# Kernel tuning notes

Hardware: AMD Instinct MI355X
Metric: run time of the kernel (lower is better)

The kernel has to match this reference:

```python
import jax, jax.numpy as jnp
import numpy as np

N = 50000        # num_nodes
E = 200000       # num_edges
NODE_IN = 16
EDGE_IN = 8
H = 128          # hidden_dim (also per-head channels in GATConv)
HEADS = 4
L = 3            # num_layers
EPS = 1e-5
NEG_SLOPE = 0.2  # PyG GATConv default


def layer_norm(x, g, b):
    mu = jnp.mean(x, axis=-1, keepdims=True)
    v = jnp.var(x, axis=-1, keepdims=True)
    return (x - mu) * jax.lax.rsqrt(v + EPS) * g + b


def batch_norm_eval(x, g, b, rm, rv):
    return (x - rm) * jax.lax.rsqrt(rv + EPS) * g + b


def gat_layer(x, src, dst, W, a_src, a_dst, bias):
    # x: [N, H] -> per-head features [N, HEADS, H]
    xh = (x @ W).reshape(N, HEADS, H)
    al_src = jnp.sum(xh * a_src, axis=-1)  # [N, HEADS]
    al_dst = jnp.sum(xh * a_dst, axis=-1)  # [N, HEADS]
    alpha = jax.nn.leaky_relu(al_src[src] + al_dst[dst], NEG_SLOPE)  # [E', HEADS]
    # segment softmax over edges grouped by destination node
    m = jax.ops.segment_max(alpha, dst, num_segments=N)
    e = jnp.exp(alpha - m[dst])
    s = jax.ops.segment_sum(e, dst, num_segments=N)
    a = e / (s[dst] + 1e-16)
    msg = xh[src] * a[:, :, None]                 # [E', HEADS, H]
    out = jax.ops.segment_sum(msg, dst, num_segments=N)  # [N, HEADS, H]
    return jnp.mean(out, axis=1) + bias           # concat=False -> head mean


def setup_inputs() -> dict:
    key = jax.random.key(0)
    ks = jax.random.split(key, 24)
    s = 0.1
    inp = {
        "x": jax.random.normal(ks[0], (N, NODE_IN), jnp.float32),
        "edge_index": jax.random.randint(ks[1], (2, E), 0, N, jnp.int32),
        "edge_attr": jax.random.normal(ks[2], (E, EDGE_IN), jnp.float32),
        "shock_mask_nodes": jax.random.randint(ks[3], (N,), 0, 2, jnp.int32),
        # node encoder
        "enc_w": jax.random.normal(ks[4], (NODE_IN + 2, H), jnp.float32) * s,
        "enc_b": jnp.zeros((H,), jnp.float32),
        "enc_ln_g": jnp.ones((H,), jnp.float32),
        "enc_ln_b": jnp.zeros((H,), jnp.float32),
        # GAT layers (stacked over L)
        "gat_w": jax.random.normal(ks[5], (L, H, HEADS * H), jnp.float32) * s,
        "gat_att_src": jax.random.normal(ks[6], (L, HEADS, H), jnp.float32) * s,
        "gat_att_dst": jax.random.normal(ks[7], (L, HEADS, H), jnp.float32) * s,
        "gat_bias": jnp.zeros((L, H), jnp.float32),
        # BatchNorm (eval mode: running stats)
        "bn_g": jnp.ones((L, H), jnp.float32),
        "bn_b": jnp.zeros((L, H), jnp.float32),
        "bn_mean": jax.random.normal(ks[8], (L, H), jnp.float32) * 0.01,
        "bn_var": jnp.ones((L, H), jnp.float32),
        # edge MLP: (2H + EDGE_IN) -> H -> H//2 -> 1
        "em1_w": jax.random.normal(ks[9], (2 * H + EDGE_IN, H), jnp.float32) * s,
        "em1_b": jnp.zeros((H,), jnp.float32),
        "em_ln_g": jnp.ones((H,), jnp.float32),
        "em_ln_b": jnp.zeros((H,), jnp.float32),
        "em2_w": jax.random.normal(ks[10], (H, H // 2), jnp.float32) * s,
        "em2_b": jnp.zeros((H // 2,), jnp.float32),
        "em3_w": jax.random.normal(ks[11], (H // 2, 1), jnp.float32) * s,
        "em3_b": jnp.zeros((1,), jnp.float32),
    }
    return inp


def reference(x, edge_index, edge_attr, shock_mask_nodes,
              enc_w, enc_b, enc_ln_g, enc_ln_b,
              gat_w, gat_att_src, gat_att_dst, gat_bias,
              bn_g, bn_b, bn_mean, bn_var,
              em1_w, em1_b, em_ln_g, em_ln_b,
              em2_w, em2_b, em3_w, em3_b):
    src, dst = edge_index[0], edge_index[1]
    shock = shock_mask_nodes.astype(jnp.float32)[:, None]  # [N,1]
    # downstream indicator: scatter_add shock[src] into tgt, binarize
    down = jax.ops.segment_sum(shock[src, 0], dst, num_segments=N)
    down = (down > 0).astype(jnp.float32)[:, None]
    xa = jnp.concatenate([x, shock, down], axis=1)  # [N, NODE_IN+2]
    # node encoder (dropout off in eval)
    h = jax.nn.relu(layer_norm(xa @ enc_w + enc_b, enc_ln_g, enc_ln_b))
    # add self loops once (PyG GATConv default add_self_loops=True)
    loop = jnp.arange(N, dtype=src.dtype)
    src_sl = jnp.concatenate([src, loop])
    dst_sl = jnp.concatenate([dst, loop])
    for i in range(L):
        h = gat_layer(h, src_sl, dst_sl, gat_w[i], gat_att_src[i], gat_att_dst[i], gat_bias[i])
        h = batch_norm_eval(h, bn_g[i], bn_b[i], bn_mean[i], bn_var[i])
        if i < L - 1:
            h = jax.nn.relu(h)
    # edge predictor (note: source uses raw edge_attr, not augmented)
    edge_input = jnp.concatenate([h[src], h[dst], edge_attr], axis=1)  # [E, 2H+EDGE_IN]
    z = jax.nn.relu(layer_norm(edge_input @ em1_w + em1_b, em_ln_g, em_ln_b))
    z = jax.nn.relu(z @ em2_w + em2_b)
    delta = (z @ em3_w + em3_b)[:, 0]  # [E]
    return delta
```

## Files before the change

kernel.cpp:

```cpp
#include <hip/hip_runtime.h>
#include <hip/hip_bf16.h>


#define N_NODES 50000
#define N_EDGES 200000
#define ETOT    (N_EDGES + N_NODES)
#define HID     128
#define LN_EPS  1e-5f
#define NEG     0.2f

typedef __hip_bfloat16 bf16;
typedef __attribute__((ext_vector_type(8))) short v8s;
typedef __attribute__((ext_vector_type(4))) float v4f;
#define MFMA(a, b, c) __builtin_amdgcn_mfma_f32_16x16x32_bf16(a, b, c, 0, 0, 0)

__device__ __forceinline__ float b2f(unsigned short s) {
    return __uint_as_float(((unsigned int)s) << 16);
}
__device__ __forceinline__ unsigned short f2b(float f) {
    __hip_bfloat16 h = __float2bfloat16(f);
    return *reinterpret_cast<unsigned short*>(&h);
}
__device__ __forceinline__ unsigned int pack2(float a, float b) {
    return (unsigned int)f2b(a) | ((unsigned int)f2b(b) << 16);
}
__device__ __forceinline__ float pread(const void* p, size_t i, int isbf) {
    if (isbf) return b2f(((const unsigned short*)p)[i]);
    return ((const float*)p)[i];
}

__global__ void k_fill(float* out, int n, float v) {
    int i = blockIdx.x * blockDim.x + threadIdx.x;
    if (i < n) out[i] = v;
}

__global__ void k_detect(const unsigned short* __restrict__ xbuf,
                         int* __restrict__ flag) {
    int sane = 0;
    for (int j = threadIdx.x; j < 4096; j += 64) {
        unsigned short v = xbuf[2 * j];
        int e = (v >> 7) & 0xFF;
        if (v == 0 || (e > 96 && e < 160)) sane++;
    }
    for (int off = 32; off > 0; off >>= 1) sane += __shfl_down(sane, off);
    if (threadIdx.x == 0) flag[0] = (sane * 10 >= 4096 * 9) ? 1 : 0;
}

struct PrepArgs {
    const void *encw, *encb, *enlg, *enlb, *gatw, *asrc, *adst, *bias,
               *bng, *bnb, *bnm, *bnv, *em1w, *em1b, *emlg, *emlb,
               *em2w, *em2b, *em3w, *em3b;
};
#define PREP_ITEMS (150000 + 8193 + 1024 + 196608 + 32768 + 8192)
__global__ void k_prep(PrepArgs a, float* __restrict__ pool,
                       unsigned short* __restrict__ gwt,
                       unsigned short* __restrict__ uvt,
                       unsigned short* __restrict__ w2t,
                       float* __restrict__ down, int* __restrict__ deg,
                       int* __restrict__ fill, const int* __restrict__ flag) {
    int i = blockIdx.x * 256 + threadIdx.x;
    int bf = flag[0];
    if (i < 150000) {
        int which = i / 50000, idx = i - which * 50000;
        if (which == 0) down[idx] = 0.f;
        else if (which == 1) deg[idx] = 0;
        else fill[idx] = 0;
        return;
    }
    i -= 150000;
    if (i < 8193) {
        const void* s; int off;
        if      (i < 2304) { s = a.encw; off = 0;    }
        else if (i < 2432) { s = a.encb; off = 2304; }
        else if (i < 2560) { s = a.enlg; off = 2432; }
        else if (i < 2688) { s = a.enlb; off = 2560; }
        else if (i < 4224) { s = a.asrc; off = 2688; }
        else if (i < 5760) { s = a.adst; off = 4224; }
        else if (i < 6144) { s = a.bias; off = 5760; }
        else if (i < 6528) { s = a.bng;  off = 6144; }
        else if (i < 6912) { s = a.bnb;  off = 6528; }
        else if (i < 7296) { s = a.bnm;  off = 6912; }
        else if (i < 7680) { s = a.bnv;  off = 7296; }
        else if (i < 7808) { s = a.em1b; off = 7680; }
        else if (i < 7936) { s = a.emlg; off = 7808; }
        else if (i < 8064) { s = a.emlb; off = 7936; }
        else if (i < 8128) { s = a.em2b; off = 8064; }
        else if (i < 8192) { s = a.em3w; off = 8128; }
        else               { s = a.em3b; off = 8192; }
        pool[i] = pread(s, i - off, bf);
        return;
    }
    i -= 8193;
    if (i < 1024) {
        int k = i >> 7, c = i & 127;
        pool[8200 + i] = pread(a.em1w, (size_t)(256 + k) * 128 + c, bf);
        return;
    }
    i -= 1024;
    if (i < 196608) {
        int L = i >> 16, rem = i & 65535, n = rem >> 7, k = rem & 127;
        gwt[i] = f2b(pread(a.gatw, (size_t)L * 65536 + (size_t)k * 512 + n, bf));
        return;
    }
    i -= 196608;
    if (i < 32768) {
        int n = i >> 7, k = i & 127;
        float v = (n < 128) ? pread(a.em1w, (size_t)k * 128 + n, bf)
                            : pread(a.em1w, (size_t)(128 + k) * 128 + (n - 128), bf);
        uvt[i] = f2b(v);
        return;
    }
    i -= 32768;
    if (i < 8192) {
        int n = i >> 7, k = i & 127;
        w2t[i] = f2b(pread(a.em2w, (size_t)k * 64 + n, bf));
    }
}

__global__ void k_graph(const int* __restrict__ ei, const int* __restrict__ shock,
                        float* __restrict__ down, int* __restrict__ deg) {
    int e = blockIdx.x * blockDim.x + threadIdx.x;
    if (e < ETOT) {
        int d = (e < N_EDGES) ? ei[N_EDGES + e] : (e - N_EDGES);
        atomicAdd(&deg[d], 1);
        if (e < N_EDGES && shock[ei[e]] != 0) down[d] = 1.f;
    }
}

__global__ __launch_bounds__(1024) void k_scan(
        const int* __restrict__ deg, int* __restrict__ row_start) {
    __shared__ int wsum[16];
    __shared__ int wexcl[16];
    const int PER = 49;
    int t = threadIdx.x, lane = t & 63, wid = t >> 6;
    int base = t * PER;
    int tot = 0;
    for (int i = 0; i < PER; i++) {
        int idx = base + i;
        if (idx < N_NODES) tot += deg[idx];
    }
    int inc = tot;
#pragma unroll
    for (int off = 1; off < 64; off <<= 1) {
        int v = __shfl_up(inc, off);
        if (lane >= off) inc += v;
    }
    if (lane == 63) wsum[wid] = inc;
    __syncthreads();
    if (wid == 0) {
        int wv = (lane < 16) ? wsum[lane] : 0;
        int winc = wv;
#pragma unroll
        for (int off = 1; off < 16; off <<= 1) {
            int v = __shfl_up(winc, off);
            if (lane >= off) winc += v;
        }
        if (lane < 16) wexcl[lane] = winc - wv;
    }
    __syncthreads();
    int run = wexcl[wid] + (inc - tot);
    for (int i = 0; i < PER; i++) {
        int idx = base + i;
        if (idx < N_NODES) {
            row_start[idx] = run;
            run += deg[idx];
        }
    }
    if (t == 0) row_start[N_NODES] = ETOT;
}

__global__ void k_csr(const int* __restrict__ ei, const int* __restrict__ row_start,
                      int* __restrict__ fill, int* __restrict__ csr_src) {
    int e = blockIdx.x * blockDim.x + threadIdx.x;
    if (e < ETOT) {
        int s, d;
        if (e < N_EDGES) { s = ei[e]; d = ei[N_EDGES + e]; }
        else             { s = e - N_EDGES; d = s; }
        int pos = row_start[d] + atomicAdd(&fill[d], 1);
        csr_src[pos] = s;
    }
}

__global__ __launch_bounds__(256) void k_encoder(
        const void* __restrict__ xraw, const int* __restrict__ flag,
        const int* __restrict__ shock, const float* __restrict__ down,
        const float* __restrict__ enc_w, const float* __restrict__ enc_b,
        const float* __restrict__ ln_g, const float* __restrict__ ln_b,
        unsigned short* __restrict__ h) {
    __shared__ float sw[2304];
    __shared__ float sp[384];
    int t = threadIdx.x;
    for (int i = t; i < 2304; i += 256) sw[i] = enc_w[i];
    if (t < 128)      sp[t] = enc_b[t];
    else if (t < 256) sp[t] = ln_g[t - 128];
    if (t < 128)      sp[256 + t] = ln_b[t];
    __syncthreads();

    int w = t >> 6, l = t & 63;
    int n = blockIdx.x * 4 + w;
    int bf = flag[0];
    int c0 = 2 * l, c1 = c0 + 1;

    float xv = (l < 16) ? pread(xraw, (size_t)n * 16 + l, bf) : 0.f;
    float xs = (float)shock[n];
    float xd = down[n];

    float a0 = sp[c0], a1 = sp[c1];
#pragma unroll
    for (int k = 0; k < 16; k++) {
        float xk = __shfl(xv, k);
        a0 = fmaf(xk, sw[k * HID + c0], a0);
        a1 = fmaf(xk, sw[k * HID + c1], a1);
    }
    a0 = fmaf(xs, sw[16 * HID + c0], a0); a1 = fmaf(xs, sw[16 * HID + c1], a1);
    a0 = fmaf(xd, sw[17 * HID + c0], a0); a1 = fmaf(xd, sw[17 * HID + c1], a1);

    float s = a0 + a1, q = a0 * a0 + a1 * a1;
#pragma unroll
    for (int off = 1; off < 64; off <<= 1) {
        s += __shfl_xor(s, off);
        q += __shfl_xor(q, off);
    }
    float mu = s * (1.f / 128.f);
    float var = q * (1.f / 128.f) - mu * mu;
    float rstd = rsqrtf(var + LN_EPS);
    float v0 = fmaxf((a0 - mu) * rstd * sp[128 + c0] + sp[256 + c0], 0.f);
    float v1 = fmaxf((a1 - mu) * rstd * sp[128 + c1] + sp[256 + c1], 0.f);
    *(unsigned int*)&h[(size_t)n * HID + c0] = pack2(v0, v1);
}

__global__ __launch_bounds__(256, 4) void k_gemm(
        const unsigned short* __restrict__ A, const unsigned short* __restrict__ Wt,
        const float* __restrict__ asrc, const float* __restrict__ adst,
        unsigned short* __restrict__ C,
        float* __restrict__ al_s, float* __restrict__ al_d) {
    __shared__ __align__(16) unsigned short As[64 * 136];
    __shared__ float alp[64][4][2];
    int t = threadIdx.x;
    int lane = t & 63, w = t >> 6, l15 = lane & 15, q = lane >> 4;
    int m0 = blockIdx.x * 64, n0 = blockIdx.y * 128, head = blockIdx.y;
    int c0 = n0 + w * 32 + 2 * l15, c1 = c0 + 1;

    v8s b[2][4];
#pragma unroll
    for (int nt = 0; nt < 2; nt++)
#pragma unroll
        for (int kt = 0; kt < 4; kt++)
            b[nt][kt] = *(const v8s*)&Wt[(size_t)(c0 + nt) * 128 + kt * 32 + q * 8];
#pragma unroll
    for (int it = 0; it < 4; it++) {
        int c = t + it * 256;
        int row = c >> 4, ch = c & 15;
        v8s val = {0, 0, 0, 0, 0, 0, 0, 0};
        if (m0 + row < N_NODES)
            val = *(const v8s*)&A[(size_t)(m0 + row) * 128 + ch * 8];
        *(v8s*)&As[row * 136 + ch * 8] = val;
    }
    __syncthreads();

    v4f acc[4][2] = {};
#pragma unroll
    for (int kt = 0; kt < 4; kt++)
#pragma unroll
        for (int mt = 0; mt < 4; mt++) {
            v8s a = *(const v8s*)&As[(mt * 16 + l15) * 136 + kt * 32 + q * 8];
            acc[mt][0] = MFMA(a, b[0][kt], acc[mt][0]);
            acc[mt][1] = MFMA(a, b[1][kt], acc[mt][1]);
        }
#pragma unroll
    for (int mt = 0; mt < 4; mt++)
#pragma unroll
        for (int r = 0; r < 4; r++) {
            int node = m0 + mt * 16 + q * 4 + r;
            if (node < N_NODES)
                *(unsigned int*)&C[(size_t)node * 512 + c0] =
                    pack2(acc[mt][0][r], acc[mt][1][r]);
        }

    float ps0 = asrc[c0], ps1 = asrc[c1];
    float pd0 = adst[c0], pd1 = adst[c1];
#pragma unroll
    for (int mt = 0; mt < 4; mt++)
#pragma unroll
        for (int r = 0; r < 4; r++) {
            float vs = acc[mt][0][r] * ps0 + acc[mt][1][r] * ps1;
            float vd = acc[mt][0][r] * pd0 + acc[mt][1][r] * pd1;
#pragma unroll
            for (int off = 1; off < 16; off <<= 1) {
                vs += __shfl_xor(vs, off);
                vd += __shfl_xor(vd, off);
            }
            if (l15 == 0) {
                alp[mt * 16 + q * 4 + r][w][0] = vs;
                alp[mt * 16 + q * 4 + r][w][1] = vd;
            }
        }
    __syncthreads();
    if (t < 64) {
        int node = m0 + t;
        if (node < N_NODES) {
            float ss = alp[t][0][0] + alp[t][1][0] + alp[t][2][0] + alp[t][3][0];
            float sd = alp[t][0][1] + alp[t][1][1] + alp[t][2][1] + alp[t][3][1];
            al_s[node * 4 + head] = ss;
            al_d[node * 4 + head] = sd;
        }
    }
}

__global__ __launch_bounds__(256) void k_aggregate(
        const unsigned short* __restrict__ xh, const float* __restrict__ al_src,
        const float* __restrict__ al_dst,
        const int* __restrict__ row_start, const int* __restrict__ csr_src,
        const float* __restrict__ bias,
        const float* __restrict__ bn_g, const float* __restrict__ bn_b,
        const float* __restrict__ bn_m, const float* __restrict__ bn_v,
        unsigned short* __restrict__ h, int relu_flag) {
    int w = threadIdx.x >> 6, l = threadIdx.x & 63;
    int n = blockIdx.x * 4 + w;
    int hh = l >> 4, c8 = l & 15;
    int r0 = row_start[n], r1 = row_start[n + 1];
    float ad = al_dst[n * 4 + hh];
    float sh = 0.f;
    float acc[8] = {};
    for (int j = r0; j < r1; j++) {
        int s = csr_src[j];
        float a = al_src[s * 4 + hh] + ad;
        a = (a >= 0.f) ? a : NEG * a;
        float we = __expf(a);
        sh += we;
        v8s row = *(const v8s*)&xh[(size_t)s * 512 + l * 8];
#pragma unroll
        for (int i = 0; i < 8; i++)
            acc[i] = fmaf(we, b2f((unsigned short)row[i]), acc[i]);
    }
    float inv = 1.f / (sh + 1e-16f);
#pragma unroll
    for (int i = 0; i < 8; i++) {
        acc[i] *= inv;
        acc[i] += __shfl_xor(acc[i], 16);
        acc[i] += __shfl_xor(acc[i], 32);
    }
    if (hh == 0) {
        int cbase = c8 * 8;
        short o[8];
#pragma unroll
        for (int i = 0; i < 8; i++) {
            int c = cbase + i;
            float v = 0.25f * acc[i] + bias[c];
            v = (v - bn_m[c]) * rsqrtf(bn_v[c] + LN_EPS) * bn_g[c] + bn_b[c];
            if (relu_flag) v = fmaxf(v, 0.f);
            o[i] = (short)f2b(v);
        }
        *(v8s*)&h[(size_t)n * 128 + cbase] = *(const v8s*)o;
    }
}

__global__ __launch_bounds__(256, 4) void k_uvgemm(
        const unsigned short* __restrict__ A, const unsigned short* __restrict__ Wt,
        unsigned short* __restrict__ UV) {
    __shared__ __align__(16) unsigned short As[64 * 136];
    int t = threadIdx.x;
    int lane = t & 63, w = t >> 6, l15 = lane & 15, q = lane >> 4;
    int m0 = blockIdx.x * 64, n0 = blockIdx.y * 128;
    int c0 = n0 + w * 32 + 2 * l15;

    v8s b[2][4];
#pragma unroll
    for (int nt = 0; nt < 2; nt++)
#pragma unroll
        for (int kt = 0; kt < 4; kt++)
            b[nt][kt] = *(const v8s*)&Wt[(size_t)(c0 + nt) * 128 + kt * 32 + q * 8];
#pragma unroll
    for (int it = 0; it < 4; it++) {
        int c = t + it * 256;
        int row = c >> 4, ch = c & 15;
        v8s val = {0, 0, 0, 0, 0, 0, 0, 0};
        if (m0 + row < N_NODES)
            val = *(const v8s*)&A[(size_t)(m0 + row) * 128 + ch * 8];
        *(v8s*)&As[row * 136 + ch * 8] = val;
    }
    __syncthreads();

    v4f acc[4][2] = {};
#pragma unroll
    for (int kt = 0; kt < 4; kt++)
#pragma unroll
        for (int mt = 0; mt < 4; mt++) {
            v8s a = *(const v8s*)&As[(mt * 16 + l15) * 136 + kt * 32 + q * 8];
            acc[mt][0] = MFMA(a, b[0][kt], acc[mt][0]);
            acc[mt][1] = MFMA(a, b[1][kt], acc[mt][1]);
        }
#pragma unroll
    for (int mt = 0; mt < 4; mt++)
#pragma unroll
        for (int r = 0; r < 4; r++) {
            int node = m0 + mt * 16 + q * 4 + r;
            if (node < N_NODES)
                *(unsigned int*)&UV[(size_t)node * 256 + c0] =
                    pack2(acc[mt][0][r], acc[mt][1][r]);
        }
}

__global__ __launch_bounds__(256) void k_edgemlp2(
        const unsigned short* __restrict__ UV, const int* __restrict__ ei,
        const void* __restrict__ eraw, const int* __restrict__ flag,
        const float* __restrict__ w1e, const float* __restrict__ em1b,
        const float* __restrict__ lng, const float* __restrict__ lnb,
        const unsigned short* __restrict__ w2t, const float* __restrict__ em2b,
        const float* __restrict__ em3w, const float* __restrict__ em3b,
        float* __restrict__ out) {
    __shared__ __align__(16) unsigned short za[64 * 136];
    __shared__ float w1e_s[1024];
    __shared__ unsigned short ea_s[64 * 8];
    __shared__ int idx_s[128];
    __shared__ float part[4][64];

    int t = threadIdx.x;
    int lane = t & 63, w = t >> 6, l15 = lane & 15, q = lane >> 4;
    int e0 = blockIdx.x * 64;
    int bf = flag[0];

    for (int i = t; i < 1024; i += 256) w1e_s[i] = w1e[i];
    if (t < 64) {
        idx_s[t * 2]     = ei[e0 + t];
        idx_s[t * 2 + 1] = ei[N_EDGES + e0 + t];
        if (bf) {
            *(v8s*)&ea_s[t * 8] =
                *(const v8s*)((const unsigned short*)eraw + (size_t)(e0 + t) * 8);
        } else {
            short tmp[8];
#pragma unroll
            for (int j = 0; j < 8; j++)
                tmp[j] = (short)f2b(((const float*)eraw)[(size_t)(e0 + t) * 8 + j]);
            *(v8s*)&ea_s[t * 8] = *(const v8s*)tmp;
        }
    }
    __syncthreads();

    int c0 = 2 * lane, c1 = c0 + 1;
    float bc0 = em1b[c0], bc1 = em1b[c1];
    float lg0 = lng[c0], lg1 = lng[c1], lb0 = lnb[c0], lb1 = lnb[c1];

    int el0 = w * 16;
    unsigned int u = *(const unsigned int*)&UV[(size_t)idx_s[el0 * 2] * 256 + c0];
    unsigned int v = *(const unsigned int*)&UV[(size_t)idx_s[el0 * 2 + 1] * 256 + 128 + c0];
#pragma unroll 1
    for (int i = 0; i < 16; i++) {
        int el = w * 16 + i;
        unsigned int uc = u, vc = v;
        if (i < 15) {
            int el2 = el + 1;
            u = *(const unsigned int*)&UV[(size_t)idx_s[el2 * 2] * 256 + c0];
            v = *(const unsigned int*)&UV[(size_t)idx_s[el2 * 2 + 1] * 256 + 128 + c0];
        }
        float e0t = 0.f, e1t = 0.f;
#pragma unroll
        for (int k = 0; k < 8; k++) {
            float eak = b2f(ea_s[el * 8 + k]);
            e0t = fmaf(eak, w1e_s[k * 128 + c0], e0t);
            e1t = fmaf(eak, w1e_s[k * 128 + c1], e1t);
        }
        float z0 = b2f(uc & 0xffff) + b2f(vc & 0xffff) + e0t + bc0;
        float z1 = b2f(uc >> 16) + b2f(vc >> 16) + e1t + bc1;
        float s = z0 + z1, qq = z0 * z0 + z1 * z1;
#pragma unroll
        for (int off = 1; off < 64; off <<= 1) {
            s  += __shfl_xor(s, off);
            qq += __shfl_xor(qq, off);
        }
        float mu = s * (1.f / 128.f);
        float var = qq * (1.f / 128.f) - mu * mu;
        float rstd = rsqrtf(var + LN_EPS);
        float y0 = fmaxf((z0 - mu) * rstd * lg0 + lb0, 0.f);
        float y1 = fmaxf((z1 - mu) * rstd * lg1 + lb1, 0.f);
        *(unsigned int*)&za[el * 136 + c0] = pack2(y0, y1);
    }
    __syncthreads();

    v8s b2[4];
#pragma unroll
    for (int kt = 0; kt < 4; kt++)
        b2[kt] = *(const v8s*)&w2t[(size_t)(w * 16 + l15) * 128 + kt * 32 + q * 8];
    v4f acc2[4] = {};
#pragma unroll
    for (int kt = 0; kt < 4; kt++)
#pragma unroll
        for (int mt = 0; mt < 4; mt++) {
            v8s a = *(const v8s*)&za[(mt * 16 + l15) * 136 + kt * 32 + q * 8];
            acc2[mt] = MFMA(a, b2[kt], acc2[mt]);
        }

    {
        int col = w * 16 + l15;
        float b2c = em2b[col], w3c = em3w[col];
#pragma unroll
        for (int mt = 0; mt < 4; mt++)
#pragma unroll
            for (int r = 0; r < 4; r++) {
                float vv = fmaxf(acc2[mt][r] + b2c, 0.f) * w3c;
#pragma unroll
                for (int off = 1; off < 16; off <<= 1) vv += __shfl_xor(vv, off);
                if (l15 == 0) part[w][mt * 16 + q * 4 + r] = vv;
            }
    }
    __syncthreads();
    if (t < 64)
        out[e0 + t] = part[0][t] + part[1][t] + part[2][t] + part[3][t]
                    + em3b[0];
}

extern "C" __attribute__((visibility("default")))
void kernel_launch(void* const* d_in, const int* in_sizes, int n_in,
                   void* d_out, int out_size, void* d_ws, size_t ws_size,
                   hipStream_t stream) {
    float* out = (float*)d_out;

    static const int EXP_SIZES[24] = {
        800000, 400000, 1600000, 50000, 2304, 128, 128, 128,
        196608, 1536, 1536, 384, 384, 384, 384, 384,
        33792, 128, 128, 128, 8192, 64, 64, 1};
    bool ok = (n_in == 24) && (out_size == N_EDGES);
    if (ok) for (int i = 0; i < 24; i++) ok = ok && (in_sizes[i] == EXP_SIZES[i]);
    if (!ok) {
        k_fill<<<(out_size + 255) / 256, 256, 0, stream>>>(out, out_size, 4.0f);
        return;
    }
    if (ws_size < (size_t)68000000) {
        k_fill<<<(out_size + 255) / 256, 256, 0, stream>>>(out, out_size, 8.0f);
        return;
    }

    const int* ei    = (const int*)d_in[1];
    const int* shock = (const int*)d_in[3];

    char* ws = (char*)d_ws;
    unsigned short* h_bf  = (unsigned short*)(ws + 0);
    unsigned short* xh    = (unsigned short*)(ws + 12800000);
    unsigned short* UV    = xh;
    float* al_s    = (float*)(ws + 64000000);
    float* al_d    = (float*)(ws + 64800000);
    float* down    = (float*)(ws + 65600000);
    int*   deg     = (int*)  (ws + 65800000);
    int*   row_st  = (int*)  (ws + 66000000);
    int*   fill    = (int*)  (ws + 66200064);
    int*   csr_src = (int*)  (ws + 66400064);
    int*   flag    = (int*)  (ws + 67400064);
    unsigned short* gwt = (unsigned short*)(ws + 67400128);
    unsigned short* uvt = (unsigned short*)(ws + 67793344);
    unsigned short* w2t = (unsigned short*)(ws + 67858880);
    float* pool    = (float*)(ws + 67875264);

    float* cencw = pool + 0;    float* cencb = pool + 2304;
    float* cenlg = pool + 2432; float* cenlb = pool + 2560;
    float* casrc = pool + 2688; float* cadst = pool + 4224;
    float* cbias = pool + 5760; float* cbng  = pool + 6144;
    float* cbnb  = pool + 6528; float* cbnm  = pool + 6912;
    float* cbnv  = pool + 7296; float* cem1b = pool + 7680;
    float* cemlg = pool + 7808; float* cemlb = pool + 7936;
    float* cem2b = pool + 8064; float* cem3w = pool + 8128;
    float* cem3b = pool + 8192;
    float* w1e   = pool + 8200;

    k_detect<<<1, 64, 0, stream>>>((const unsigned short*)d_in[0], flag);

    PrepArgs pa;
    pa.encw = d_in[4];  pa.encb = d_in[5];  pa.enlg = d_in[6];  pa.enlb = d_in[7];
    pa.gatw = d_in[8];  pa.asrc = d_in[9];  pa.adst = d_in[10]; pa.bias = d_in[11];
    pa.bng  = d_in[12]; pa.bnb  = d_in[13]; pa.bnm  = d_in[14]; pa.bnv  = d_in[15];
    pa.em1w = d_in[16]; pa.em1b = d_in[17]; pa.emlg = d_in[18]; pa.emlb = d_in[19];
    pa.em2w = d_in[20]; pa.em2b = d_in[21]; pa.em3w = d_in[22]; pa.em3b = d_in[23];
    k_prep<<<(PREP_ITEMS + 255) / 256, 256, 0, stream>>>(
        pa, pool, gwt, uvt, w2t, down, deg, fill, flag);

    k_graph<<<(ETOT + 255) / 256, 256, 0, stream>>>(ei, shock, down, deg);
    k_scan<<<1, 1024, 0, stream>>>(deg, row_st);
    k_csr<<<(ETOT + 255) / 256, 256, 0, stream>>>(ei, row_st, fill, csr_src);
    k_encoder<<<N_NODES / 4, 256, 0, stream>>>(
        d_in[0], flag, shock, down, cencw, cencb, cenlg, cenlb, h_bf);
    for (int i = 0; i < 3; i++) {
        k_gemm<<<dim3(782, 4), 256, 0, stream>>>(
            h_bf, gwt + (size_t)i * 65536, casrc + i * 512, cadst + i * 512,
            xh, al_s, al_d);
        k_aggregate<<<N_NODES / 4, 256, 0, stream>>>(
            xh, al_s, al_d, row_st, csr_src,
            cbias + i * 128, cbng + i * 128, cbnb + i * 128,
            cbnm + i * 128, cbnv + i * 128, h_bf, (i < 2) ? 1 : 0);
    }
    k_uvgemm<<<dim3(782, 2), 256, 0, stream>>>(h_bf, uvt, UV);
    k_edgemlp2<<<N_EDGES / 64, 256, 0, stream>>>(
        UV, ei, d_in[2], flag, w1e, cem1b, cemlg, cemlb,
        w2t, cem2b, cem3w, cem3b, out);
}
```

Measured before the change: 572.0 us.

## Replace single-block degree scan with two-pass multi-block scan

The exclusive prefix sum over node degrees used to run in one 1024-thread block, with each thread handling 49 strided elements serially. It is now split into two kernels over 196 blocks. The first writes per-block sums, and the second has each block add up the preceding block sums and then do a block-local scan. This spreads a serial, latency-bound kernel across the GPU, at the cost of one extra launch and a small bsum buffer in the workspace.

```diff
diff --git a/kernel.cpp b/kernel.cpp
--- a/kernel.cpp
+++ b/kernel.cpp
@@ -8,6 +8,7 @@
 #define HID     128
 #define LN_EPS  1e-5f
 #define NEG     0.2f
+#define NSB     196
 
 typedef __hip_bfloat16 bf16;
 typedef __attribute__((ext_vector_type(8))) short v8s;
@@ -127,46 +128,46 @@
     }
 }
 
-__global__ __launch_bounds__(1024) void k_scan(
-        const int* __restrict__ deg, int* __restrict__ row_start) {
-    __shared__ int wsum[16];
-    __shared__ int wexcl[16];
-    const int PER = 49;
-    int t = threadIdx.x, lane = t & 63, wid = t >> 6;
-    int base = t * PER;
-    int tot = 0;
-    for (int i = 0; i < PER; i++) {
-        int idx = base + i;
-        if (idx < N_NODES) tot += deg[idx];
-    }
-    int inc = tot;
+__global__ __launch_bounds__(256) void k_scan1(
+        const int* __restrict__ deg, int* __restrict__ bsum) {
+    __shared__ int red[4];
+    int b = blockIdx.x, t = threadIdx.x, lane = t & 63, w = t >> 6;
+    int idx = b * 256 + t;
+    int v = (idx < N_NODES) ? deg[idx] : 0;
+#pragma unroll
+    for (int off = 1; off < 64; off <<= 1) v += __shfl_xor(v, off);
+    if (lane == 0) red[w] = v;
+    __syncthreads();
+    if (t == 0) bsum[b] = red[0] + red[1] + red[2] + red[3];
+}
+
+__global__ __launch_bounds__(256) void k_scan2(
+        const int* __restrict__ deg, const int* __restrict__ bsum,
+        int* __restrict__ row_start) {
+    __shared__ int red[4];
+    __shared__ int wsum[4];
+    int b = blockIdx.x, t = threadIdx.x, lane = t & 63, w = t >> 6;
+    int pv = (t < b) ? bsum[t] : 0;
+    int sm = pv;
+#pragma unroll
+    for (int off = 1; off < 64; off <<= 1) sm += __shfl_xor(sm, off);
+    if (lane == 0) red[w] = sm;
+    int idx = b * 256 + t;
+    int v = (idx < N_NODES) ? deg[idx] : 0;
+    int inc = v;
 #pragma unroll
     for (int off = 1; off < 64; off <<= 1) {
-        int v = __shfl_up(inc, off);
-        if (lane >= off) inc += v;
-    }
-    if (lane == 63) wsum[wid] = inc;
-    __syncthreads();
-    if (wid == 0) {
-        int wv = (lane < 16) ? wsum[lane] : 0;
-        int winc = wv;
-#pragma unroll
-        for (int off = 1; off < 16; off <<= 1) {
-            int v = __shfl_up(winc, off);
-            if (lane >= off) winc += v;
-        }
-        if (lane < 16) wexcl[lane] = winc - wv;
-    }
-    __syncthreads();
-    int run = wexcl[wid] + (inc - tot);
-    for (int i = 0; i < PER; i++) {
-        int idx = base + i;
-        if (idx < N_NODES) {
-            row_start[idx] = run;
-            run += deg[idx];
-        }
-    }
-    if (t == 0) row_start[N_NODES] = ETOT;
+        int u = __shfl_up(inc, off);
+        if (lane >= off) inc += u;
+    }
+    if (lane == 63) wsum[w] = inc;
+    __syncthreads();
+    int boff = red[0] + red[1] + red[2] + red[3];
+    int wo = 0;
+#pragma unroll
+    for (int i = 0; i < 4; i++) if (i < w) wo += wsum[i];
+    if (idx < N_NODES) row_start[idx] = boff + wo + (inc - v);
+    if (b == 0 && t == 0) row_start[N_NODES] = ETOT;
 }
 
 __global__ void k_csr(const int* __restrict__ ei, const int* __restrict__ row_start,
@@ -549,6 +550,7 @@
     unsigned short* uvt = (unsigned short*)(ws + 67793344);
     unsigned short* w2t = (unsigned short*)(ws + 67858880);
     float* pool    = (float*)(ws + 67875264);
+    int*   bsum    = (int*)  (ws + 67912160);
 
     float* cencw = pool + 0;    float* cencb = pool + 2304;
     float* cenlg = pool + 2432; float* cenlb = pool + 2560;
@@ -573,7 +575,8 @@
         pa, pool, gwt, uvt, w2t, down, deg, fill, flag);
 
     k_graph<<<(ETOT + 255) / 256, 256, 0, stream>>>(ei, shock, down, deg);
-    k_scan<<<1, 1024, 0, stream>>>(deg, row_st);
+    k_scan1<<<NSB, 256, 0, stream>>>(deg, bsum);
+    k_scan2<<<NSB, 256, 0, stream>>>(deg, bsum, row_st);
     k_csr<<<(ETOT + 255) / 256, 256, 0, stream>>>(ei, row_st, fill, csr_src);
     k_encoder<<<N_NODES / 4, 256, 0, stream>>>(
         d_in[0], flag, shock, down, cencw, cencb, cenlg, cenlb, h_bf);
```

Result: faster. 484.8 us (-15.2%).
